# Kernel optimization log

Measured on AMD Instinct MI355X. Metric: run time of the kernel, lower is better.

## Reference

```python
import math
import jax, jax.numpy as jnp
import numpy as np

B, T, DIM = 1, 2048, 2048
NH, NKV = 32, 8
HD = DIM // NH  # 64
REP = NH // NKV  # 4


def _rope(x):
    # x: [b, h, t, d]; rotates as in the torch module (half-split, concat form)
    d = x.shape[-1]
    half = d // 2
    t = x.shape[2]
    freqs = jnp.arange(half, dtype=x.dtype) / max(half, 1)
    angles = jnp.arange(t, dtype=x.dtype)[:, None] * freqs[None, :]  # [t, half]
    sin = jnp.sin(angles)[None, None]  # [1,1,t,half]
    cos = jnp.cos(angles)[None, None]
    x1, x2 = x[..., :half], x[..., half:]
    return jnp.concatenate([x1 * cos - x2 * sin, x1 * sin + x2 * cos], axis=-1)


def setup_inputs() -> dict:
    key = jax.random.key(0)
    k1, k2, k3 = jax.random.split(key, 3)
    sd = 1.0 / math.sqrt(DIM)
    return {
        "x": jax.random.normal(k1, (B, T, DIM), dtype=jnp.float32),
        "Wqkv": jax.random.normal(k2, ((NH + 2 * NKV) * HD, DIM), dtype=jnp.float32) * sd,
        "Wproj": jax.random.normal(k3, (DIM, DIM), dtype=jnp.float32) * sd,
        "q_gain": jnp.ones((NH,), dtype=jnp.float32),
        "attn_temp": jnp.ones((NH,), dtype=jnp.float32),
    }


def reference(x, Wqkv, Wproj, q_gain, attn_temp):
    b, t, c = x.shape
    qkv = x @ Wqkv.T  # [b, t, (NH+2*NKV)*HD]
    q, k, v = jnp.split(qkv, [NH * HD, (NH + NKV) * HD], axis=2)
    q = q.reshape(b, t, NH, HD).transpose(0, 2, 1, 3)   # [b, NH, t, HD]
    k = k.reshape(b, t, NKV, HD).transpose(0, 2, 1, 3)  # [b, NKV, t, HD]
    v = v.reshape(b, t, NKV, HD).transpose(0, 2, 1, 3)
    # GQA expand (repeat_interleave along head axis)
    k = jnp.repeat(k, REP, axis=1)  # [b, NH, t, HD]
    v = jnp.repeat(v, REP, axis=1)
    q = _rope(q)
    k = _rope(k)
    q = q * (q_gain * attn_temp)[None, :, None, None]
    scale = 1.0 / math.sqrt(HD)
    scores = jnp.einsum('bhqd,bhkd->bhqk', q, k) * scale
    causal = jnp.tril(jnp.ones((t, t), dtype=bool))
    scores = jnp.where(causal[None, None], scores, jnp.finfo(scores.dtype).min)
    attn = jax.nn.softmax(scores, axis=-1)
    y = jnp.einsum('bhqk,bhkd->bhqd', attn, v)  # [b, NH, t, HD]
    y = y.transpose(0, 2, 1, 3).reshape(b, t, c)
    return y @ Wproj.T
```

## Files before the change

### kernel.cpp

```cpp
#include <hip/hip_runtime.h>
#include <hip/hip_bf16.h>
#include <math.h>

typedef unsigned short u16;
typedef __attribute__((ext_vector_type(8))) short short8;
typedef __attribute__((ext_vector_type(4))) float f32x4;
typedef __attribute__((ext_vector_type(4))) unsigned short u16x4;
typedef __attribute__((ext_vector_type(4))) unsigned int u32x4;

#define DEVI static __device__ __forceinline__

DEVI u16 f2bf(float f){
  union { float f; unsigned u; } c; c.f = f;
  unsigned r = (c.u + 0x7fffu + ((c.u >> 16) & 1u)) >> 16;
  return (u16)r;
}

DEVI unsigned cvtpk(float lo, float hi){
  unsigned r;
  asm("v_cvt_pk_bf16_f32 %0, %1, %2" : "=v"(r) : "v"(lo), "v"(hi));
  return r;
}

DEVI void async16(const void* g, void* l){
  __builtin_amdgcn_global_load_lds(
    (const __attribute__((address_space(1))) unsigned int*)g,
    (__attribute__((address_space(3))) unsigned int*)l, 16, 0, 0);
}

#define WAIT_BAR(N) asm volatile("s_waitcnt vmcnt(" #N ") lgkmcnt(0)\n\ts_barrier" ::: "memory")

#define ACHUNK(r, g) (((r) << 2) | (((g) + ((r) >> 1)) & 3))
#define KCH(r, g) (((r) << 3) | (((g) + ((r) >> 1)) & 7))

__global__ __launch_bounds__(256) void cvt3(const float4* __restrict__ x,
                                            const float4* __restrict__ wq,
                                            const float4* __restrict__ wp,
                                            u16* __restrict__ xb,
                                            u16* __restrict__ wqb,
                                            u16* __restrict__ wpb){
  int i = blockIdx.x * 256 + threadIdx.x;
  const float4* s; u16* d; int off;
  if (i < 1048576)      { s = x;  d = xb;  off = i; }
  else if (i < 2621440) { s = wq; d = wqb; off = i - 1048576; }
  else                  { s = wp; d = wpb; off = i - 2621440; }
  float4 v = s[off];
  u16x4 o;
  o.x = f2bf(v.x); o.y = f2bf(v.y); o.z = f2bf(v.z); o.w = f2bf(v.w);
  *(u16x4*)(d + (size_t)off * 4) = o;
}

__global__ __launch_bounds__(256) void gemm_qkv(const u16* __restrict__ A,
                                                const u16* __restrict__ B,
                                                const float* __restrict__ qg,
                                                const float* __restrict__ at_,
                                                u16* __restrict__ qb,
                                                u16* __restrict__ kb,
                                                u16* __restrict__ vT){
  const int K = 2048;
  __shared__ __align__(16) u16 As[4][4096];
  __shared__ __align__(16) u16 Bs[4][4096];
  const int bid = blockIdx.x;
  const int xcd = bid & 7, pos = bid >> 3;
  const int xm = xcd & 1, xn = xcd >> 1;
  const int mIdx = xm * 8 + (pos & 7);
  const int nIdx = xn * 6 + (pos >> 3);
  const int tid  = threadIdx.x;
  const int lane = tid & 63, wid = tid >> 6;
  const int wr = wid >> 1, wc = wid & 1;
  const int fr = lane & 15, fg = lane >> 4;
  const int mBase = mIdx * 128, nBase = nIdx * 128;

  f32x4 acc[4][4];
  for (int m = 0; m < 4; ++m)
    for (int n = 0; n < 4; ++n)
      for (int e = 0; e < 4; ++e) acc[m][n][e] = 0.f;

  const int c0 = tid, c1 = tid + 256;
  const int p0 = c0 >> 2, q0 = ((c0 & 3) - (p0 >> 1)) & 3;
  const int p1 = c1 >> 2, q1 = ((c1 & 3) - (p1 >> 1)) & 3;
  const u16* Ab = A + (size_t)mBase * K;
  const u16* Bb = B + (size_t)nBase * K;

  int ca[4], cb[4];
#pragma unroll
  for (int m = 0; m < 4; ++m){ const int r = wr * 64 + m * 16 + fr; ca[m] = ACHUNK(r, fg); }
#pragma unroll
  for (int n = 0; n < 4; ++n){ const int r = wc * 64 + n * 16 + fr; cb[n] = ACHUNK(r, fg); }

#define STAGE_QKV(kt, b) do {                                        \
    const int kO_ = (kt) * 32;                                       \
    async16(Ab + (size_t)p0 * K + kO_ + q0 * 8, As[b] + c0 * 8);     \
    async16(Ab + (size_t)p1 * K + kO_ + q1 * 8, As[b] + c1 * 8);     \
    async16(Bb + (size_t)p0 * K + kO_ + q0 * 8, Bs[b] + c0 * 8);     \
    async16(Bb + (size_t)p1 * K + kO_ + q1 * 8, Bs[b] + c1 * 8);     \
  } while (0)

  STAGE_QKV(0, 0); STAGE_QKV(1, 1); STAGE_QKV(2, 2);

  const int nk = 64;
#pragma unroll 1
  for (int kt = 0; kt < nk; ++kt){
    const int cur = kt & 3;
    if (kt < nk - 2)       WAIT_BAR(8);
    else if (kt == nk - 2) WAIT_BAR(4);
    else                   WAIT_BAR(0);
    if (kt + 3 < nk) STAGE_QKV(kt + 3, (kt + 3) & 3);
    short8 a[4], b[4];
#pragma unroll
    for (int m = 0; m < 4; ++m)
      a[m] = *(const short8*)(As[cur] + ca[m] * 8);
#pragma unroll
    for (int n = 0; n < 4; ++n)
      b[n] = *(const short8*)(Bs[cur] + cb[n] * 8);
    __builtin_amdgcn_s_setprio(1);
#pragma unroll
    for (int m = 0; m < 4; ++m)
#pragma unroll
      for (int n = 0; n < 4; ++n)
        acc[m][n] = __builtin_amdgcn_mfma_f32_16x16x32_bf16(a[m], b[n], acc[m][n], 0, 0, 0);
    __builtin_amdgcn_s_setprio(0);
  }
#undef STAGE_QKV

  const int nb64 = nIdx * 2 + wc;
  if (nb64 < 40){
    const bool isq = nb64 < 32;
    const int h = isq ? nb64 : (nb64 - 32);
    const float gsc = isq ? (qg[h] * at_[h] * 0.125f) : 1.0f;
    u16* dst = isq ? qb : kb;
#pragma unroll
    for (int m = 0; m < 4; ++m)
#pragma unroll
      for (int e = 0; e < 4; ++e){
        const int t = mBase + wr * 64 + m * 16 + fg * 4 + e;
        const float ft = (float)t;
#pragma unroll
        for (int np = 0; np < 2; ++np){
          const int d = np * 16 + fr;
          const float ang = ft * ((float)d * 0.03125f);
          float sn, cs; sincosf(ang, &sn, &cs);
          const float x1 = acc[m][np][e], x2 = acc[m][np + 2][e];
          u16* base = dst + ((size_t)h * 2048 + t) * 64 + d;
          base[0]  = f2bf((x1 * cs - x2 * sn) * gsc);
          base[32] = f2bf((x1 * sn + x2 * cs) * gsc);
        }
      }
  } else {
    const int h = nb64 - 40;
#pragma unroll
    for (int m = 0; m < 4; ++m){
      const int t0 = mBase + wr * 64 + m * 16 + fg * 4;
#pragma unroll
      for (int n = 0; n < 4; ++n){
        const int d = n * 16 + fr;
        u16x4 pk;
#pragma unroll
        for (int e = 0; e < 4; ++e) pk[e] = f2bf(acc[m][n][e]);
        *(u16x4*)(vT + ((size_t)h * 64 + d) * 2048 + t0) = pk;
      }
    }
  }
}

__global__ __launch_bounds__(256) void attn_fwd(const u16* __restrict__ qb,
                                                const u16* __restrict__ kb,
                                                const u16* __restrict__ vT,
                                                u16* __restrict__ yb){
  const int bx = blockIdx.x, h = blockIdx.y;
  const int hk = h >> 2;
  const int tid = threadIdx.x;
  const int lane = tid & 63, wid = tid >> 6;
  const int fr = lane & 15, fg = lane >> 4;

  __shared__ __align__(16) u16 Ks[2][4096];
  __shared__ __align__(16) u16 Vs[2][4096];

  const u16* kbh = kb + (size_t)hk * 2048 * 64;
  const u16* vTh = vT + (size_t)hk * 64 * 2048;

  const int c0 = tid, c1 = tid + 256;
  const int p0 = c0 >> 3, q0 = ((c0 & 7) - (p0 >> 1)) & 7;
  const int p1 = c1 >> 3, q1 = ((c1 & 7) - (p1 >> 1)) & 7;
  const int pr0 = ((p0 >> 5) << 5) | (((p0 >> 2) & 3) << 3) | (((p0 >> 4) & 1) << 2) | (p0 & 3);
  const int pr1 = ((p1 >> 5) << 5) | (((p1 >> 2) & 3) << 3) | (((p1 >> 4) & 1) << 2) | (p1 & 3);

  int ck[2][4], cv[2][4];
#pragma unroll
  for (int kc = 0; kc < 2; ++kc)
#pragma unroll
    for (int cf = 0; cf < 4; ++cf){
      ck[kc][cf] = KCH(cf * 16 + fr, kc * 4 + fg);
      cv[kc][cf] = KCH(cf * 16 + fr, kc * 4 + fg);
    }

#pragma unroll 1
  for (int seg = 0; seg < 2; ++seg){
    const int qt = seg ? (31 - bx) : bx;
    const int nt = qt + 1;
    const int qrow0 = qt * 64 + wid * 16;
    const int q = qrow0 + fr;

    short8 qf[2];
    {
      const u16* qp = qb + ((size_t)h * 2048 + q) * 64 + fg * 8;
      qf[0] = *(const short8*)(qp);
      qf[1] = *(const short8*)(qp + 32);
    }

    float mrow = -1e30f, lrow = 0.f;
    f32x4 o[4];
    for (int df = 0; df < 4; ++df)
      for (int e = 0; e < 4; ++e) o[df][e] = 0.f;

    async16(kbh + (size_t)pr0 * 64 + q0 * 8,        Ks[0] + (size_t)c0 * 8);
    async16(kbh + (size_t)pr1 * 64 + q1 * 8,        Ks[0] + (size_t)c1 * 8);
    async16(vTh + (size_t)p0 * 2048 + q0 * 8,       Vs[0] + (size_t)c0 * 8);
    async16(vTh + (size_t)p1 * 2048 + q1 * 8,       Vs[0] + (size_t)c1 * 8);

#pragma unroll 1
    for (int kt = 0; kt < nt; ++kt){
      const int cur = kt & 1;
      __syncthreads();
      if (kt + 1 < nt){
        const int nxt = cur ^ 1;
        const size_t kO = (size_t)(kt + 1) * 64;
        async16(kbh + (kO + pr0) * 64 + q0 * 8,       Ks[nxt] + (size_t)c0 * 8);
        async16(kbh + (kO + pr1) * 64 + q1 * 8,       Ks[nxt] + (size_t)c1 * 8);
        async16(vTh + (size_t)p0 * 2048 + kO + q0 * 8, Vs[nxt] + (size_t)c0 * 8);
        async16(vTh + (size_t)p1 * 2048 + kO + q1 * 8, Vs[nxt] + (size_t)c1 * 8);
      }
      const u16* Kb = Ks[cur];
      const u16* Vb = Vs[cur];

      f32x4 s[4];
      __builtin_amdgcn_s_setprio(1);
#pragma unroll
      for (int cf = 0; cf < 4; ++cf){
        for (int e = 0; e < 4; ++e) s[cf][e] = 0.f;
#pragma unroll
        for (int kc = 0; kc < 2; ++kc){
          short8 kf = *(const short8*)(Kb + ck[kc][cf] * 8);
          s[cf] = __builtin_amdgcn_mfma_f32_16x16x32_bf16(kf, qf[kc], s[cf], 0, 0, 0);
        }
      }
      __builtin_amdgcn_s_setprio(0);

      if (kt * 64 + 63 > qrow0){
#pragma unroll
        for (int cf = 0; cf < 4; ++cf){
          const int kb0 = kt * 64 + (cf >> 1) * 32 + (cf & 1) * 4 + fg * 8;
#pragma unroll
          for (int r = 0; r < 4; ++r)
            if (kb0 + r > q) s[cf][r] = -1e30f;
        }
      }

      float m0 = fmaxf(fmaxf(s[0][0], s[0][1]), fmaxf(s[0][2], s[0][3]));
      float m1 = fmaxf(fmaxf(s[1][0], s[1][1]), fmaxf(s[1][2], s[1][3]));
      float m2 = fmaxf(fmaxf(s[2][0], s[2][1]), fmaxf(s[2][2], s[2][3]));
      float m3 = fmaxf(fmaxf(s[3][0], s[3][1]), fmaxf(s[3][2], s[3][3]));
      float mt = fmaxf(fmaxf(m0, m1), fmaxf(m2, m3));
      mt = fmaxf(mt, __shfl_xor(mt, 16));
      mt = fmaxf(mt, __shfl_xor(mt, 32));
      if (!__all(mt <= mrow + 8.f)){
        const float mn = fmaxf(mrow, mt);
        const float al = __expf(mrow - mn);
        lrow *= al;
#pragma unroll
        for (int df = 0; df < 4; ++df)
#pragma unroll
          for (int e = 0; e < 4; ++e) o[df][e] *= al;
        mrow = mn;
      }
      float rs = 0.f;
#pragma unroll
      for (int cf = 0; cf < 4; ++cf){
#pragma unroll
        for (int r = 0; r < 4; ++r){
          s[cf][r] = __expf(s[cf][r] - mrow);
          rs += s[cf][r];
        }
      }
      rs += __shfl_xor(rs, 16);
      rs += __shfl_xor(rs, 32);
      lrow += rs;

      union { u32x4 u; short8 s8; } pb0, pb1;
      pb0.u[0] = cvtpk(s[0][0], s[0][1]); pb0.u[1] = cvtpk(s[0][2], s[0][3]);
      pb0.u[2] = cvtpk(s[1][0], s[1][1]); pb0.u[3] = cvtpk(s[1][2], s[1][3]);
      pb1.u[0] = cvtpk(s[2][0], s[2][1]); pb1.u[1] = cvtpk(s[2][2], s[2][3]);
      pb1.u[2] = cvtpk(s[3][0], s[3][1]); pb1.u[3] = cvtpk(s[3][2], s[3][3]);

      __builtin_amdgcn_s_setprio(1);
#pragma unroll
      for (int df = 0; df < 4; ++df){
        short8 v0 = *(const short8*)(Vb + cv[0][df] * 8);
        short8 v1 = *(const short8*)(Vb + cv[1][df] * 8);
        o[df] = __builtin_amdgcn_mfma_f32_16x16x32_bf16(v0, pb0.s8, o[df], 0, 0, 0);
        o[df] = __builtin_amdgcn_mfma_f32_16x16x32_bf16(v1, pb1.s8, o[df], 0, 0, 0);
      }
      __builtin_amdgcn_s_setprio(0);
    }
    __syncthreads();

    const float inv = 1.f / lrow;
#pragma unroll
    for (int df = 0; df < 4; ++df){
      u16x4 pk;
#pragma unroll
      for (int e = 0; e < 4; ++e) pk[e] = f2bf(o[df][e] * inv);
      *(u16x4*)(yb + (size_t)q * 2048 + h * 64 + df * 16 + fg * 4) = pk;
    }
  }
}

__global__ __launch_bounds__(256) void gemm_bt(const u16* __restrict__ A,
                                               const u16* __restrict__ B,
                                               float* __restrict__ C,
                                               int M, int N, int K){
  __shared__ __align__(16) u16 As[4][4096];
  __shared__ __align__(16) u16 Bs[4][4096];
  const int bid = blockIdx.x;
  const int xcd = bid & 7, pos = bid >> 3;
  const int xm = xcd & 1, xn = xcd >> 1;
  const int mIdx = xm * 8 + (pos & 7);
  const int nIdx = xn * 4 + (pos >> 3);
  const int tid  = threadIdx.x;
  const int lane = tid & 63, wid = tid >> 6;
  const int wr = wid >> 1, wc = wid & 1;
  const int fr = lane & 15, fg = lane >> 4;
  const int mBase = mIdx * 128, nBase = nIdx * 128;

  f32x4 acc[4][4];
  for (int m = 0; m < 4; ++m)
    for (int n = 0; n < 4; ++n)
      for (int e = 0; e < 4; ++e) acc[m][n][e] = 0.f;

  const int c0 = tid, c1 = tid + 256;
  const int p0 = c0 >> 2, q0 = ((c0 & 3) - (p0 >> 1)) & 3;
  const int p1 = c1 >> 2, q1 = ((c1 & 3) - (p1 >> 1)) & 3;
  const u16* Ab = A + (size_t)mBase * K;
  const u16* Bb = B + (size_t)nBase * K;

  int ca[4], cb[4];
#pragma unroll
  for (int m = 0; m < 4; ++m){ const int r = wr * 64 + m * 16 + fr; ca[m] = ACHUNK(r, fg); }
#pragma unroll
  for (int n = 0; n < 4; ++n){ const int r = wc * 64 + n * 16 + fr; cb[n] = ACHUNK(r, fg); }

#define STAGE_BT(kt, b) do {                                         \
    const int kO_ = (kt) * 32;                                       \
    async16(Ab + (size_t)p0 * K + kO_ + q0 * 8, As[b] + c0 * 8);     \
    async16(Ab + (size_t)p1 * K + kO_ + q1 * 8, As[b] + c1 * 8);     \
    async16(Bb + (size_t)p0 * K + kO_ + q0 * 8, Bs[b] + c0 * 8);     \
    async16(Bb + (size_t)p1 * K + kO_ + q1 * 8, Bs[b] + c1 * 8);     \
  } while (0)

  STAGE_BT(0, 0); STAGE_BT(1, 1); STAGE_BT(2, 2);

  const int nk = K >> 5;
#pragma unroll 1
  for (int kt = 0; kt < nk; ++kt){
    const int cur = kt & 3;
    if (kt < nk - 2)       WAIT_BAR(8);
    else if (kt == nk - 2) WAIT_BAR(4);
    else                   WAIT_BAR(0);
    if (kt + 3 < nk) STAGE_BT(kt + 3, (kt + 3) & 3);
    short8 a[4], b[4];
#pragma unroll
    for (int m = 0; m < 4; ++m)
      a[m] = *(const short8*)(As[cur] + ca[m] * 8);
#pragma unroll
    for (int n = 0; n < 4; ++n)
      b[n] = *(const short8*)(Bs[cur] + cb[n] * 8);
    __builtin_amdgcn_s_setprio(1);
#pragma unroll
    for (int m = 0; m < 4; ++m)
#pragma unroll
      for (int n = 0; n < 4; ++n)
        acc[m][n] = __builtin_amdgcn_mfma_f32_16x16x32_bf16(a[m], b[n], acc[m][n], 0, 0, 0);
    __builtin_amdgcn_s_setprio(0);
  }
#undef STAGE_BT

  for (int m = 0; m < 4; ++m){
    const int row = mBase + wr * 64 + m * 16 + fg * 4;
    for (int n = 0; n < 4; ++n){
      const int col = nBase + wc * 64 + n * 16 + fr;
      for (int e = 0; e < 4; ++e)
        C[(size_t)(row + e) * N + col] = acc[m][n][e];
    }
  }
}

extern "C" void kernel_launch(void* const* d_in, const int* in_sizes, int n_in,
                              void* d_out, int out_size, void* d_ws, size_t ws_size,
                              hipStream_t stream){
  (void)in_sizes; (void)n_in; (void)out_size; (void)ws_size;
  const float* x     = (const float*)d_in[0];
  const float* Wqkv  = (const float*)d_in[1];
  const float* Wproj = (const float*)d_in[2];
  const float* qg    = (const float*)d_in[3];
  const float* at    = (const float*)d_in[4];
  float* out = (float*)d_out;

  u16* xb     = (u16*)d_ws;
  u16* wqkvb  = xb + 4194304;
  u16* wprojb = wqkvb + 6291456;
  u16* qbuf   = wprojb + 4194304;
  u16* kbuf   = qbuf + 4194304;
  u16* vTb    = kbuf + 1048576;
  u16* ybuf   = vTb + 1048576;

  cvt3<<<14336, 256, 0, stream>>>((const float4*)x, (const float4*)Wqkv,
                                  (const float4*)Wproj, xb, wqkvb, wprojb);
  gemm_qkv<<<384, 256, 0, stream>>>(xb, wqkvb, qg, at, qbuf, kbuf, vTb);
  attn_fwd<<<dim3(16, 32), 256, 0, stream>>>(qbuf, kbuf, vTb, ybuf);
  gemm_bt<<<256, 256, 0, stream>>>(ybuf, wprojb, out, 2048, 2048, 2048);
}
```

Before: 151.2 us.

## Share K/V tiles across two GQA heads per 512-thread attention block

Each attention block now runs 8 waves covering two query heads that share one KV head, so each K/V tile is loaded into LDS once and used by both heads. The grid drops to 256 blocks, and block IDs are remapped so consecutive heads sharing a KV head land on the same XCD for better L2 locality. This halves K/V global traffic and async copies per head, at the cost of fewer, larger blocks, which may hurt occupancy and load balance across CUs. The duplicated cv offset table is also dropped in favour of reusing ck.

```diff
diff --git a/kernel.cpp b/kernel.cpp
--- a/kernel.cpp
+++ b/kernel.cpp
@@ -163,15 +163,19 @@
   }
 }
 
-__global__ __launch_bounds__(256) void attn_fwd(const u16* __restrict__ qb,
+__global__ __launch_bounds__(512) void attn_fwd(const u16* __restrict__ qb,
                                                 const u16* __restrict__ kb,
                                                 const u16* __restrict__ vT,
                                                 u16* __restrict__ yb){
-  const int bx = blockIdx.x, h = blockIdx.y;
-  const int hk = h >> 2;
+  const int bid = blockIdx.x;
+  const int xcd = bid & 7, pos = bid >> 3;
+  const int hp = (xcd << 1) | (pos >> 4);
+  const int bx = pos & 15;
+  const int hk = hp >> 1;
   const int tid = threadIdx.x;
   const int lane = tid & 63, wid = tid >> 6;
   const int fr = lane & 15, fg = lane >> 4;
+  const int h = hp * 2 + (wid >> 2);
 
   __shared__ __align__(16) u16 Ks[2][4096];
   __shared__ __align__(16) u16 Vs[2][4096];
@@ -179,26 +183,22 @@
   const u16* kbh = kb + (size_t)hk * 2048 * 64;
   const u16* vTh = vT + (size_t)hk * 64 * 2048;
 
-  const int c0 = tid, c1 = tid + 256;
+  const int c0 = tid;
   const int p0 = c0 >> 3, q0 = ((c0 & 7) - (p0 >> 1)) & 7;
-  const int p1 = c1 >> 3, q1 = ((c1 & 7) - (p1 >> 1)) & 7;
   const int pr0 = ((p0 >> 5) << 5) | (((p0 >> 2) & 3) << 3) | (((p0 >> 4) & 1) << 2) | (p0 & 3);
-  const int pr1 = ((p1 >> 5) << 5) | (((p1 >> 2) & 3) << 3) | (((p1 >> 4) & 1) << 2) | (p1 & 3);
-
-  int ck[2][4], cv[2][4];
+
+  int ck[2][4];
 #pragma unroll
   for (int kc = 0; kc < 2; ++kc)
 #pragma unroll
-    for (int cf = 0; cf < 4; ++cf){
+    for (int cf = 0; cf < 4; ++cf)
       ck[kc][cf] = KCH(cf * 16 + fr, kc * 4 + fg);
-      cv[kc][cf] = KCH(cf * 16 + fr, kc * 4 + fg);
-    }
 
 #pragma unroll 1
   for (int seg = 0; seg < 2; ++seg){
     const int qt = seg ? (31 - bx) : bx;
     const int nt = qt + 1;
-    const int qrow0 = qt * 64 + wid * 16;
+    const int qrow0 = qt * 64 + (wid & 3) * 16;
     const int q = qrow0 + fr;
 
     short8 qf[2];
@@ -213,10 +213,8 @@
     for (int df = 0; df < 4; ++df)
       for (int e = 0; e < 4; ++e) o[df][e] = 0.f;
 
-    async16(kbh + (size_t)pr0 * 64 + q0 * 8,        Ks[0] + (size_t)c0 * 8);
-    async16(kbh + (size_t)pr1 * 64 + q1 * 8,        Ks[0] + (size_t)c1 * 8);
-    async16(vTh + (size_t)p0 * 2048 + q0 * 8,       Vs[0] + (size_t)c0 * 8);
-    async16(vTh + (size_t)p1 * 2048 + q1 * 8,       Vs[0] + (size_t)c1 * 8);
+    async16(kbh + (size_t)pr0 * 64 + q0 * 8,  Ks[0] + (size_t)c0 * 8);
+    async16(vTh + (size_t)p0 * 2048 + q0 * 8, Vs[0] + (size_t)c0 * 8);
 
 #pragma unroll 1
     for (int kt = 0; kt < nt; ++kt){
@@ -225,10 +223,8 @@
       if (kt + 1 < nt){
         const int nxt = cur ^ 1;
         const size_t kO = (size_t)(kt + 1) * 64;
-        async16(kbh + (kO + pr0) * 64 + q0 * 8,       Ks[nxt] + (size_t)c0 * 8);
-        async16(kbh + (kO + pr1) * 64 + q1 * 8,       Ks[nxt] + (size_t)c1 * 8);
+        async16(kbh + (kO + pr0) * 64 + q0 * 8,        Ks[nxt] + (size_t)c0 * 8);
         async16(vTh + (size_t)p0 * 2048 + kO + q0 * 8, Vs[nxt] + (size_t)c0 * 8);
-        async16(vTh + (size_t)p1 * 2048 + kO + q1 * 8, Vs[nxt] + (size_t)c1 * 8);
       }
       const u16* Kb = Ks[cur];
       const u16* Vb = Vs[cur];
@@ -295,8 +291,8 @@
       __builtin_amdgcn_s_setprio(1);
 #pragma unroll
       for (int df = 0; df < 4; ++df){
-        short8 v0 = *(const short8*)(Vb + cv[0][df] * 8);
-        short8 v1 = *(const short8*)(Vb + cv[1][df] * 8);
+        short8 v0 = *(const short8*)(Vb + ck[0][df] * 8);
+        short8 v1 = *(const short8*)(Vb + ck[1][df] * 8);
         o[df] = __builtin_amdgcn_mfma_f32_16x16x32_bf16(v0, pb0.s8, o[df], 0, 0, 0);
         o[df] = __builtin_amdgcn_mfma_f32_16x16x32_bf16(v1, pb1.s8, o[df], 0, 0, 0);
       }
@@ -416,6 +412,6 @@
   cvt3<<<14336, 256, 0, stream>>>((const float4*)x, (const float4*)Wqkv,
                                   (const float4*)Wproj, xb, wqkvb, wprojb);
   gemm_qkv<<<384, 256, 0, stream>>>(xb, wqkvb, qg, at, qbuf, kbuf, vTb);
-  attn_fwd<<<dim3(16, 32), 256, 0, stream>>>(qbuf, kbuf, vTb, ybuf);
+  attn_fwd<<<256, 512, 0, stream>>>(qbuf, kbuf, vTb, ybuf);
   gemm_bt<<<256, 256, 0, stream>>>(ybuf, wprojb, out, 2048, 2048, 2048);
 }
```

After: 149.8 us. No clear change (-1.0%).
